# Kernel tuning notes

Hardware: AMD Instinct MI355X
Metric: run time of the kernel (lower is better)

## Reference

```python
import jax, jax.numpy as jnp
import numpy as np

N = 100000   # nodes
E = 600000   # edges
D = 128      # d_model
R = 200      # num_relations


def setup_inputs() -> dict:
    key = jax.random.key(0)
    ks = jax.random.split(key, 12)
    def nrm(k, shape, scale=0.02):
        return jax.random.normal(k, shape, jnp.float32) * scale
    return dict(
        node_features=jax.random.normal(ks[0], (N, D), jnp.float32),
        edge_index=jax.random.randint(ks[1], (2, E), 0, N),
        edge_type=jax.random.randint(ks[2], (E,), 0, R),
        rel_embed=nrm(ks[3], (R, D)),
        msg_w1=nrm(ks[4], (2 * D, D)), msg_b1=jnp.zeros((D,), jnp.float32),
        msg_w2=nrm(ks[5], (D, D)), msg_b2=jnp.zeros((D,), jnp.float32),
        attn_w1=nrm(ks[6], (2 * D, D)), attn_b1=jnp.zeros((D,), jnp.float32),
        attn_w2=nrm(ks[7], (D, 1)), attn_b2=jnp.zeros((1,), jnp.float32),
        ln1_g=jnp.ones((D,), jnp.float32), ln1_b=jnp.zeros((D,), jnp.float32),
        ffn_w1=nrm(ks[8], (D, 4 * D)), ffn_b1=jnp.zeros((4 * D,), jnp.float32),
        ffn_w2=nrm(ks[9], (4 * D, D)), ffn_b2=jnp.zeros((D,), jnp.float32),
        ln2_g=jnp.ones((D,), jnp.float32), ln2_b=jnp.zeros((D,), jnp.float32),
    )


def layer_norm(x, g, b, eps=1e-5):
    mu = x.mean(-1, keepdims=True)
    var = ((x - mu) ** 2).mean(-1, keepdims=True)
    return (x - mu) * jax.lax.rsqrt(var + eps) * g + b


def reference(node_features, edge_index, edge_type, rel_embed,
              msg_w1, msg_b1, msg_w2, msg_b2,
              attn_w1, attn_b1, attn_w2, attn_b2,
              ln1_g, ln1_b, ffn_w1, ffn_b1, ffn_w2, ffn_b2,
              ln2_g, ln2_b):
    Nn = node_features.shape[0]
    src, dst = edge_index[0], edge_index[1]
    # gather + edge message MLP
    src_feat = node_features[src]              # [E, D]
    rel_feat = rel_embed[edge_type]            # [E, D]
    h = jnp.concatenate([src_feat, rel_feat], axis=-1)          # [E, 2D]
    messages = jax.nn.relu(h @ msg_w1 + msg_b1) @ msg_w2 + msg_b2  # [E, D]
    # edge attention logits
    a_in = jnp.concatenate([node_features[dst], messages], axis=-1)  # [E, 2D]
    attn_raw = (jax.nn.leaky_relu(a_in @ attn_w1 + attn_b1, 0.2) @ attn_w2 + attn_b2)[:, 0]  # [E]
    # two-pass segment softmax over destination nodes
    attn_max = jax.ops.segment_max(attn_raw, dst, num_segments=Nn)   # [N]
    attn_exp = jnp.exp(attn_raw - attn_max[dst])                      # [E]
    attn_sum = jax.ops.segment_sum(attn_exp, dst, num_segments=Nn)   # [N]
    attn_w = attn_exp / (attn_sum[dst] + 1e-8)                        # [E]
    # scatter-add weighted messages
    aggr = jax.ops.segment_sum(attn_w[:, None] * messages, dst, num_segments=Nn)  # [N, D]
    x = layer_norm(node_features + aggr, ln1_g, ln1_b)
    ffn = jax.nn.gelu(x @ ffn_w1 + ffn_b1, approximate=False) @ ffn_w2 + ffn_b2
    return layer_norm(x + ffn, ln2_g, ln2_b)
```

## Files before the change

### kernel.cpp

```cpp
#include <hip/hip_runtime.h>
#include <hip/hip_bf16.h>

#define NN 100000
#define NE 600000
#define DD 128
#define RR 200
#define SCAN_NB ((NN + 255) / 256)

typedef __attribute__((ext_vector_type(8))) short bf16x8;
typedef __attribute__((ext_vector_type(4))) float f32x4;

__device__ __forceinline__ unsigned int bfbits(float x) {
    return (unsigned int)__builtin_bit_cast(unsigned short, __float2bfloat16(x));
}
__device__ __forceinline__ unsigned int pk2(float a, float b) {
    return bfbits(a) | (bfbits(b) << 16);
}
__device__ __forceinline__ unsigned short bf16s(float x) {
    return __builtin_bit_cast(unsigned short, __float2bfloat16(x));
}
__device__ __forceinline__ float unbf(unsigned short u) {
    return __builtin_bit_cast(float, ((unsigned int)u) << 16);
}
__device__ __forceinline__ float unlo(unsigned int u) {
    return __builtin_bit_cast(float, u << 16);
}
__device__ __forceinline__ float unhi(unsigned int u) {
    return __builtin_bit_cast(float, u & 0xffff0000u);
}

__device__ __forceinline__ void gload_lds16(const void* g, void* l) {
    __builtin_amdgcn_global_load_lds(
        (const __attribute__((address_space(1))) void*)g,
        (__attribute__((address_space(3))) void*)l, 16, 0, 0);
}

__global__ void k_initc(int* __restrict__ cnt) {
    int i = blockIdx.x * 256 + threadIdx.x;
    if (i < NN) cnt[i] = 0;
}

__global__ void k_hist(const int* __restrict__ dst, int* __restrict__ cnt) {
    int e = blockIdx.x * 256 + threadIdx.x;
    if (e < NE) atomicAdd(&cnt[dst[e]], 1);
}

__global__ void k_scanA(const int* __restrict__ cnt, int* __restrict__ bsum) {
    __shared__ int red[256];
    int i = blockIdx.x * 256 + threadIdx.x;
    red[threadIdx.x] = (i < NN) ? cnt[i] : 0;
    __syncthreads();
    for (int off = 128; off >= 1; off >>= 1) {
        if (threadIdx.x < off) red[threadIdx.x] += red[threadIdx.x + off];
        __syncthreads();
    }
    if (threadIdx.x == 0) bsum[blockIdx.x] = red[0];
}

__global__ void k_scanB(int* __restrict__ bsum) {
    __shared__ int sh[512];
    int t = threadIdx.x;
    int v = (t < SCAN_NB) ? bsum[t] : 0;
    sh[t] = v;
    __syncthreads();
    for (int off = 1; off < 512; off <<= 1) {
        int add = (t >= off) ? sh[t - off] : 0;
        __syncthreads();
        sh[t] += add;
        __syncthreads();
    }
    if (t < SCAN_NB) bsum[t] = sh[t] - v;
}

__global__ void k_scanC(const int* __restrict__ cnt, const int* __restrict__ bsum,
                        int* __restrict__ row_start, int* __restrict__ cursor) {
    __shared__ int sh[256];
    int i = blockIdx.x * 256 + threadIdx.x;
    int t = threadIdx.x;
    int v = (i < NN) ? cnt[i] : 0;
    sh[t] = v;
    __syncthreads();
    for (int off = 1; off < 256; off <<= 1) {
        int add = (t >= off) ? sh[t - off] : 0;
        __syncthreads();
        sh[t] += add;
        __syncthreads();
    }
    if (i < NN) {
        int ex = bsum[blockIdx.x] + sh[t] - v;
        row_start[i] = ex;
        cursor[i] = ex;
    }
}

__global__ void k_bucket(const int* __restrict__ src, const int* __restrict__ dst,
                         const int* __restrict__ etype, int* __restrict__ cursor,
                         int* __restrict__ srcs, int* __restrict__ ets,
                         int* __restrict__ dsts) {
    int e = blockIdx.x * 256 + threadIdx.x;
    if (e < NE) {
        int d = dst[e];
        int p = atomicAdd(&cursor[d], 1);
        srcs[p] = src[e];
        ets[p]  = etype[e];
        dsts[p] = d;
    }
}

__global__ void k_prep(const float* __restrict__ nf, unsigned short* __restrict__ nfb) {
    int i = blockIdx.x * 256 + threadIdx.x;
    if (i >= NN * DD / 8) return;
    const float* sp = nf + (size_t)i * 8;
    float4 f0 = *reinterpret_cast<const float4*>(sp);
    float4 f1 = *reinterpret_cast<const float4*>(sp + 4);
    uint4 v;
    v.x = pk2(f0.x, f0.y); v.y = pk2(f0.z, f0.w);
    v.z = pk2(f1.x, f1.y); v.w = pk2(f1.z, f1.w);
    *reinterpret_cast<uint4*>(nfb + (size_t)i * 8) = v;
}

__global__ void k_relc(const float* __restrict__ rel, const float* __restrict__ mw1,
                       const float* __restrict__ mb1, unsigned short* __restrict__ relcb) {
    int idx = blockIdx.x * 256 + threadIdx.x;
    if (idx >= RR * DD) return;
    int r = idx >> 7, n = idx & 127;
    float s = mb1[n];
    for (int k = 0; k < 128; ++k)
        s = fmaf(rel[r * 128 + k], mw1[(128 + k) * 128 + n], s);
    relcb[idx] = bf16s(s);
}

__global__ void k_mwb(const float* __restrict__ mw2, const float* __restrict__ mb2,
                      const float* __restrict__ aw1,
                      float* __restrict__ mwB, float* __restrict__ zb) {
    int idx = blockIdx.x * 256 + threadIdx.x;
    if (idx < 16384) {
        int k = idx >> 7, n = idx & 127;
        float s = 0.0f;
        for (int j = 0; j < 128; ++j)
            s = fmaf(mw2[k * 128 + j], aw1[(128 + j) * 128 + n], s);
        mwB[idx] = s;
    } else if (idx < 16512) {
        int n = idx - 16384;
        float s = 0.0f;
        for (int j = 0; j < 128; ++j)
            s = fmaf(mb2[j], aw1[(128 + j) * 128 + n], s);
        zb[n] = s;
    }
}

__global__ void k_pack(const float* __restrict__ mw1, const float* __restrict__ mw2,
                       const float* __restrict__ mwB,
                       const float* __restrict__ aw1,
                       const float* __restrict__ fw1, const float* __restrict__ fw2,
                       unsigned short* __restrict__ mw1p,
                       unsigned short* __restrict__ mwCp,
                       unsigned short* __restrict__ awTp,
                       unsigned short* __restrict__ fw1p,
                       unsigned short* __restrict__ fw2p) {
    int idx = blockIdx.x * 256 + threadIdx.x;
    if (idx < 16384) {
        int i = idx & 7, l = (idx >> 3) & 63, ks = (idx >> 9) & 3, nt = idx >> 11;
        int k = ks * 32 + (l >> 4) * 8 + i, n = nt * 16 + (l & 15);
        mw1p[idx] = bf16s(mw1[k * 128 + n]);
    } else if (idx < 49152) {
        int j = idx - 16384;
        int i = j & 7, l = (j >> 3) & 63, ks = (j >> 9) & 3, nt = j >> 11;
        int k = ks * 32 + (l >> 4) * 8 + i, n = nt * 16 + (l & 15);
        mwCp[j] = bf16s((n < 128) ? mw2[k * 128 + n] : mwB[k * 128 + (n - 128)]);
    } else if (idx < 65536) {
        int j = idx - 49152;
        int i = j & 7, l = (j >> 3) & 63, ks = (j >> 9) & 3, nt = j >> 11;
        int k = ks * 32 + (l >> 4) * 8 + i, n = nt * 16 + (l & 15);
        awTp[j] = bf16s(aw1[k * 128 + n]);
    } else if (idx < 131072) {
        int j = idx - 65536;
        int i = j & 7, l = (j >> 3) & 63, ks = (j >> 9) & 3, nt = j >> 11;
        int k = ks * 32 + (l >> 4) * 8 + i, n = nt * 16 + (l & 15);
        fw1p[j] = bf16s(fw1[k * 512 + n]);
    } else if (idx < 196608) {
        int j = idx - 131072;
        int i = j & 7, l = (j >> 3) & 63, ks = (j >> 9) & 15, nt = j >> 13;
        int k = ks * 32 + (l >> 4) * 8 + i, n = nt * 16 + (l & 15);
        fw2p[j] = bf16s(fw2[k * 128 + n]);
    }
}

__global__ __launch_bounds__(256) void k_nfa(
    const unsigned short* __restrict__ nfb, const unsigned short* __restrict__ awTp,
    const float* __restrict__ ab1, unsigned short* __restrict__ nfa)
{
    __shared__ alignas(16) unsigned short XB[64 * 128];
    const int t = threadIdx.x;
    const int w = t >> 6, l = t & 63;
    const int wm = w >> 1, wn = w & 1;
    const int lm = l & 15, lk = l >> 4;
    const int lrow = l >> 4, lslot = l & 15;
    const int n0 = blockIdx.x * 64;

    #pragma unroll
    for (int it = 0; it < 4; ++it) {
        int rb = w * 16 + it * 4;
        int row = rb + lrow;
        long grow = n0 + row; if (grow >= NN) grow = NN - 1;
        int c = lslot ^ (row & 7);
        gload_lds16(nfb + grow * DD + c * 8, &XB[rb * 128]);
    }
    __syncthreads();

    f32x4 acc[2][4];
    #pragma unroll
    for (int mf = 0; mf < 2; ++mf)
        #pragma unroll
        for (int nfr = 0; nfr < 4; ++nfr) acc[mf][nfr] = (f32x4){0.f, 0.f, 0.f, 0.f};

    #pragma unroll
    for (int ks = 0; ks < 4; ++ks) {
        bf16x8 a[2];
        #pragma unroll
        for (int mf = 0; mf < 2; ++mf) {
            int m = wm * 32 + mf * 16 + lm;
            int slot = (ks * 4 + lk) ^ (m & 7);
            a[mf] = *reinterpret_cast<const bf16x8*>(&XB[m * 128 + slot * 8]);
        }
        #pragma unroll
        for (int nfr = 0; nfr < 4; ++nfr) {
            int nt = wn * 4 + nfr;
            bf16x8 b = *reinterpret_cast<const bf16x8*>(&awTp[((nt * 4 + ks) * 64 + l) * 8]);
            acc[0][nfr] = __builtin_amdgcn_mfma_f32_16x16x32_bf16(a[0], b, acc[0][nfr], 0, 0, 0);
            acc[1][nfr] = __builtin_amdgcn_mfma_f32_16x16x32_bf16(a[1], b, acc[1][nfr], 0, 0, 0);
        }
    }
    __syncthreads();

    #pragma unroll
    for (int nfr = 0; nfr < 4; ++nfr) {
        int n = wn * 64 + nfr * 16 + lm;
        float bv = ab1[n];
        #pragma unroll
        for (int mf = 0; mf < 2; ++mf)
            #pragma unroll
            for (int r = 0; r < 4; ++r) {
                int m = wm * 32 + mf * 16 + lk * 4 + r;
                XB[m * 128 + n] = bf16s(acc[mf][nfr][r] + bv);
            }
    }
    __syncthreads();

    #pragma unroll
    for (int j = 0; j < 4; ++j) {
        int q = j * 256 + t;
        int row = q >> 4, c16 = q & 15;
        if (n0 + row < NN)
            *reinterpret_cast<uint4*>(&nfa[(size_t)(n0 + row) * DD + c16 * 8]) =
                *reinterpret_cast<const uint4*>(&XB[row * 128 + c16 * 8]);
    }
}

__global__ __launch_bounds__(512) void k_edge(
    const unsigned short* __restrict__ nfb, const int* __restrict__ srcs,
    const int* __restrict__ dsts, const int* __restrict__ ets,
    const unsigned short* __restrict__ nfa, const unsigned short* __restrict__ relcb,
    const unsigned short* __restrict__ mw1p, const unsigned short* __restrict__ mwCp,
    const float* __restrict__ mb2, const float* __restrict__ zb,
    const float* __restrict__ aw2, const float* __restrict__ ab2,
    unsigned short* __restrict__ msg_out, float* __restrict__ attn_raw)
{
    __shared__ alignas(16) unsigned short S[64 * 128];
    __shared__ alignas(16) unsigned short H[64 * 128];
    __shared__ float RED[64][2];

    const int t = threadIdx.x;
    const int w = t >> 6, l = t & 63;
    const int wm = w >> 2, wn = w & 3;
    const int lm = l & 15, lk = l >> 4;
    const int lrow = l >> 4, lslot = l & 15;
    const int e0 = blockIdx.x * 64;

    #pragma unroll
    for (int it = 0; it < 2; ++it) {
        int rb = w * 8 + it * 4;
        int row = rb + lrow;
        int c = lslot ^ (row & 7);
        gload_lds16(nfb + (size_t)srcs[e0 + row] * DD + c * 8, &S[rb * 128]);
    }
    #pragma unroll
    for (int it = 0; it < 2; ++it) {
        int rb = w * 8 + it * 4;
        int row = rb + lrow;
        int c = lslot ^ (row & 7);
        gload_lds16(relcb + (size_t)ets[e0 + row] * DD + c * 8, &H[rb * 128]);
    }
    __syncthreads();

    {
        f32x4 acc[2][2];
        #pragma unroll
        for (int mf = 0; mf < 2; ++mf)
            #pragma unroll
            for (int nfr = 0; nfr < 2; ++nfr) acc[mf][nfr] = (f32x4){0.f, 0.f, 0.f, 0.f};

        #pragma unroll
        for (int ks = 0; ks < 4; ++ks) {
            bf16x8 a[2];
            #pragma unroll
            for (int mf = 0; mf < 2; ++mf) {
                int m = wm * 32 + mf * 16 + lm;
                int slot = (ks * 4 + lk) ^ (m & 7);
                a[mf] = *reinterpret_cast<const bf16x8*>(&S[m * 128 + slot * 8]);
            }
            #pragma unroll
            for (int nfr = 0; nfr < 2; ++nfr) {
                int nt = wn * 2 + nfr;
                bf16x8 b = *reinterpret_cast<const bf16x8*>(&mw1p[((nt * 4 + ks) * 64 + l) * 8]);
                acc[0][nfr] = __builtin_amdgcn_mfma_f32_16x16x32_bf16(a[0], b, acc[0][nfr], 0, 0, 0);
                acc[1][nfr] = __builtin_amdgcn_mfma_f32_16x16x32_bf16(a[1], b, acc[1][nfr], 0, 0, 0);
            }
        }
        #pragma unroll
        for (int nfr = 0; nfr < 2; ++nfr) {
            int n = (wn * 2 + nfr) * 16 + lm;
            #pragma unroll
            for (int mf = 0; mf < 2; ++mf)
                #pragma unroll
                for (int r = 0; r < 4; ++r) {
                    int m = wm * 32 + mf * 16 + lk * 4 + r;
                    int sl = m * 128 + ((n >> 3) ^ (m & 7)) * 8 + (n & 7);
                    float v = acc[mf][nfr][r] + unbf(H[sl]);
                    v = fmaxf(v, 0.0f);
                    H[sl] = bf16s(v);
                }
        }
    }
    __syncthreads();

    #pragma unroll
    for (int it = 0; it < 2; ++it) {
        int rb = w * 8 + it * 4;
        int row = rb + lrow;
        int c = lslot ^ (row & 7);
        gload_lds16(nfa + (size_t)dsts[e0 + row] * DD + c * 8, &S[rb * 128]);
    }

    f32x4 acc[2][4];
    #pragma unroll
    for (int mf = 0; mf < 2; ++mf)
        #pragma unroll
        for (int nfr = 0; nfr < 4; ++nfr) acc[mf][nfr] = (f32x4){0.f, 0.f, 0.f, 0.f};

    #pragma unroll
    for (int ks = 0; ks < 4; ++ks) {
        bf16x8 a[2];
        #pragma unroll
        for (int mf = 0; mf < 2; ++mf) {
            int m = wm * 32 + mf * 16 + lm;
            int slot = (ks * 4 + lk) ^ (m & 7);
            a[mf] = *reinterpret_cast<const bf16x8*>(&H[m * 128 + slot * 8]);
        }
        #pragma unroll
        for (int nfr = 0; nfr < 4; ++nfr) {
            int nt = wn * 4 + nfr;
            bf16x8 b = *reinterpret_cast<const bf16x8*>(&mwCp[((nt * 4 + ks) * 64 + l) * 8]);
            acc[0][nfr] = __builtin_amdgcn_mfma_f32_16x16x32_bf16(a[0], b, acc[0][nfr], 0, 0, 0);
            acc[1][nfr] = __builtin_amdgcn_mfma_f32_16x16x32_bf16(a[1], b, acc[1][nfr], 0, 0, 0);
        }
    }
    __syncthreads();

    if (wn < 2) {
        #pragma unroll
        for (int nfr = 0; nfr < 4; ++nfr) {
            int n = (wn * 4 + nfr) * 16 + lm;
            float bv = mb2[n];
            #pragma unroll
            for (int mf = 0; mf < 2; ++mf)
                #pragma unroll
                for (int r = 0; r < 4; ++r) {
                    int m = wm * 32 + mf * 16 + lk * 4 + r;
                    H[m * 128 + ((n >> 3) ^ (m & 7)) * 8 + (n & 7)] = bf16s(acc[mf][nfr][r] + bv);
                }
        }
    } else {
        float zbv[4], aw2v[4];
        #pragma unroll
        for (int nfr = 0; nfr < 4; ++nfr) {
            int nc = (wn - 2) * 64 + nfr * 16 + lm;
            zbv[nfr] = zb[nc];
            aw2v[nfr] = aw2[nc];
        }
        #pragma unroll
        for (int mf = 0; mf < 2; ++mf)
            #pragma unroll
            for (int r = 0; r < 4; ++r) {
                int m = wm * 32 + mf * 16 + lk * 4 + r;
                float s = 0.0f;
                #pragma unroll
                for (int nfr = 0; nfr < 4; ++nfr) {
                    int nc = (wn - 2) * 64 + nfr * 16 + lm;
                    float v = acc[mf][nfr][r] + zbv[nfr]
                            + unbf(S[m * 128 + ((nc >> 3) ^ (m & 7)) * 8 + (nc & 7)]);
                    v = (v > 0.0f) ? v : 0.2f * v;
                    s = fmaf(v, aw2v[nfr], s);
                }
                s += __shfl_xor(s, 1, 64);
                s += __shfl_xor(s, 2, 64);
                s += __shfl_xor(s, 4, 64);
                s += __shfl_xor(s, 8, 64);
                if (lm == 0) RED[m][wn - 2] = s;
            }
    }
    __syncthreads();

    #pragma unroll
    for (int j = 0; j < 2; ++j) {
        int q = j * 512 + t;
        int row = q >> 4, c16 = q & 15;
        int slot = c16 ^ (row & 7);
        *reinterpret_cast<uint4*>(&msg_out[(size_t)(e0 + row) * DD + c16 * 8]) =
            *reinterpret_cast<const uint4*>(&H[row * 128 + slot * 8]);
    }
    if (t < 64) {
        attn_raw[e0 + t] = RED[t][0] + RED[t][1] + ab2[0];
    }
}

__global__ __launch_bounds__(256) void k_aggr(
    const unsigned short* __restrict__ msg, const float* __restrict__ raw,
    const int* __restrict__ row_start, const int* __restrict__ cnt,
    float* __restrict__ aggr)
{
    const int l = threadIdx.x & 63;
    const int n = blockIdx.x * 4 + (threadIdx.x >> 6);
    if (n >= NN) return;
    const int rs = row_start[n], deg = cnt[n];

    float m = -INFINITY;
    for (int j = l; j < deg; j += 64) m = fmaxf(m, raw[rs + j]);
    #pragma unroll
    for (int off = 32; off >= 1; off >>= 1) m = fmaxf(m, __shfl_xor(m, off, 64));

    float s = 0.0f;
    for (int j = l; j < deg; j += 64) s += expf(raw[rs + j] - m);
    #pragma unroll
    for (int off = 32; off >= 1; off >>= 1) s += __shfl_xor(s, off, 64);
    const float rinv = 1.0f / (s + 1e-8f);

    float a0 = 0.0f, a1 = 0.0f;
    for (int j = 0; j < deg; ++j) {
        float w = expf(raw[rs + j] - m) * rinv;
        unsigned int v = *reinterpret_cast<const unsigned int*>(
            &msg[(size_t)(rs + j) * DD + l * 2]);
        a0 = fmaf(w, unlo(v), a0);
        a1 = fmaf(w, unhi(v), a1);
    }
    float2 o = {a0, a1};
    *reinterpret_cast<float2*>(&aggr[(size_t)n * DD + l * 2]) = o;
}

__global__ __launch_bounds__(512) void k_node(
    const float* __restrict__ nf, const float* __restrict__ aggr,
    const float* __restrict__ g1, const float* __restrict__ b1,
    const unsigned short* __restrict__ fw1p, const float* __restrict__ fb1,
    const unsigned short* __restrict__ fw2p, const float* __restrict__ fb2,
    const float* __restrict__ g2, const float* __restrict__ b2,
    float* __restrict__ out)
{
    __shared__ alignas(16) unsigned short XB[64 * 128];
    __shared__ alignas(16) unsigned short HB[64 * 256];

    const int t = threadIdx.x;
    const int w = t >> 6, l = t & 63;
    const int wm = w >> 2, wn = w & 3;
    const int lm = l & 15, lk = l >> 4;
    const int row = t >> 3;
    const int q = t & 7;
    const long n0 = (long)blockIdx.x * 64;
    const long rg = n0 + row;
    const long rc = (rg < NN) ? rg : (NN - 1);

    float xr[16];
    float s = 0.0f, ss = 0.0f;
    {
        const float* xp = nf + rc * DD + q * 16;
        const float* ap = aggr + rc * DD + q * 16;
        #pragma unroll
        for (int i = 0; i < 4; ++i) {
            float4 a = *reinterpret_cast<const float4*>(xp + i * 4);
            float4 b = *reinterpret_cast<const float4*>(ap + i * 4);
            float v0 = a.x + b.x, v1 = a.y + b.y, v2 = a.z + b.z, v3 = a.w + b.w;
            xr[i * 4 + 0] = v0; xr[i * 4 + 1] = v1; xr[i * 4 + 2] = v2; xr[i * 4 + 3] = v3;
            s += v0 + v1 + v2 + v3;
            ss = fmaf(v0, v0, ss); ss = fmaf(v1, v1, ss);
            ss = fmaf(v2, v2, ss); ss = fmaf(v3, v3, ss);
        }
    }
    s  += __shfl_xor(s, 1, 64);  s  += __shfl_xor(s, 2, 64);  s  += __shfl_xor(s, 4, 64);
    ss += __shfl_xor(ss, 1, 64); ss += __shfl_xor(ss, 2, 64); ss += __shfl_xor(ss, 4, 64);
    {
        float mu = s * (1.0f / DD);
        float var = ss * (1.0f / DD) - mu * mu;
        float rstd = rsqrtf(var + 1e-5f);
        #pragma unroll
        for (int i = 0; i < 4; ++i) {
            float4 gv = *reinterpret_cast<const float4*>(g1 + q * 16 + i * 4);
            float4 bv = *reinterpret_cast<const float4*>(b1 + q * 16 + i * 4);
            xr[i * 4 + 0] = (xr[i * 4 + 0] - mu) * rstd * gv.x + bv.x;
            xr[i * 4 + 1] = (xr[i * 4 + 1] - mu) * rstd * gv.y + bv.y;
            xr[i * 4 + 2] = (xr[i * 4 + 2] - mu) * rstd * gv.z + bv.z;
            xr[i * 4 + 3] = (xr[i * 4 + 3] - mu) * rstd * gv.w + bv.w;
        }
        #pragma unroll
        for (int i = 0; i < 2; ++i) {
            int c = q * 2 + i, slot = c ^ (row & 7);
            uint4 v;
            v.x = pk2(xr[i * 8 + 0], xr[i * 8 + 1]);
            v.y = pk2(xr[i * 8 + 2], xr[i * 8 + 3]);
            v.z = pk2(xr[i * 8 + 4], xr[i * 8 + 5]);
            v.w = pk2(xr[i * 8 + 6], xr[i * 8 + 7]);
            *reinterpret_cast<uint4*>(&XB[row * 128 + slot * 8]) = v;
        }
    }
    __syncthreads();

    f32x4 acc2[2][2];
    #pragma unroll
    for (int mf = 0; mf < 2; ++mf)
        #pragma unroll
        for (int nfr = 0; nfr < 2; ++nfr) acc2[mf][nfr] = (f32x4){0.f, 0.f, 0.f, 0.f};

    #pragma unroll
    for (int half = 0; half < 2; ++half) {
        f32x4 acc[2][4];
        #pragma unroll
        for (int mf = 0; mf < 2; ++mf)
            #pragma unroll
            for (int nfr = 0; nfr < 4; ++nfr) acc[mf][nfr] = (f32x4){0.f, 0.f, 0.f, 0.f};

        #pragma unroll
        for (int ks = 0; ks < 4; ++ks) {
            bf16x8 a[2];
            #pragma unroll
            for (int mf = 0; mf < 2; ++mf) {
                int m = wm * 32 + mf * 16 + lm;
                int slot = (ks * 4 + lk) ^ (m & 7);
                a[mf] = *reinterpret_cast<const bf16x8*>(&XB[m * 128 + slot * 8]);
            }
            #pragma unroll
            for (int nfr = 0; nfr < 4; ++nfr) {
                int nt = half * 16 + wn * 4 + nfr;
                bf16x8 b = *reinterpret_cast<const bf16x8*>(&fw1p[((nt * 4 + ks) * 64 + l) * 8]);
                acc[0][nfr] = __builtin_amdgcn_mfma_f32_16x16x32_bf16(a[0], b, acc[0][nfr], 0, 0, 0);
                acc[1][nfr] = __builtin_amdgcn_mfma_f32_16x16x32_bf16(a[1], b, acc[1][nfr], 0, 0, 0);
            }
        }
        #pragma unroll
        for (int nfr = 0; nfr < 4; ++nfr) {
            int nl = (wn * 4 + nfr) * 16 + lm;
            float bv = fb1[half * 256 + nl];
            #pragma unroll
            for (int mf = 0; mf < 2; ++mf)
                #pragma unroll
                for (int r = 0; r < 4; ++r) {
                    int m = wm * 32 + mf * 16 + lk * 4 + r;
                    float h = acc[mf][nfr][r] + bv;
                    float e = __expf(h * -1.702f);
                    float gvv = h * __builtin_amdgcn_rcpf(1.0f + e);
                    HB[m * 256 + (((nl >> 3) ^ (m & 7)) * 8) + (nl & 7)] = bf16s(gvv);
                }
        }
        __syncthreads();

        #pragma unroll
        for (int ks = 0; ks < 8; ++ks) {
            bf16x8 a[2];
            #pragma unroll
            for (int mf = 0; mf < 2; ++mf) {
                int m = wm * 32 + mf * 16 + lm;
                int slot = (ks * 4 + lk) ^ (m & 7);
                a[mf] = *reinterpret_cast<const bf16x8*>(&HB[m * 256 + slot * 8]);
            }
            #pragma unroll
            for (int nfr = 0; nfr < 2; ++nfr) {
                int nt = wn * 2 + nfr;
                int kg = half * 8 + ks;
                bf16x8 b = *reinterpret_cast<const bf16x8*>(&fw2p[((nt * 16 + kg) * 64 + l) * 8]);
                acc2[0][nfr] = __builtin_amdgcn_mfma_f32_16x16x32_bf16(a[0], b, acc2[0][nfr], 0, 0, 0);
                acc2[1][nfr] = __builtin_amdgcn_mfma_f32_16x16x32_bf16(a[1], b, acc2[1][nfr], 0, 0, 0);
            }
        }
        __syncthreads();
    }

    #pragma unroll
    for (int nfr = 0; nfr < 2; ++nfr) {
        int n = (wn * 2 + nfr) * 16 + lm;
        float bv = fb2[n];
        #pragma unroll
        for (int mf = 0; mf < 2; ++mf)
            #pragma unroll
            for (int r = 0; r < 4; ++r) {
                int m = wm * 32 + mf * 16 + lk * 4 + r;
                XB[m * 128 + (((n >> 3) ^ (m & 7)) * 8) + (n & 7)] = bf16s(acc2[mf][nfr][r] + bv);
            }
    }
    __syncthreads();

    float s2 = 0.0f, ss2 = 0.0f;
    #pragma unroll
    for (int i = 0; i < 2; ++i) {
        int c = q * 2 + i, slot = c ^ (row & 7);
        uint4 v = *reinterpret_cast<const uint4*>(&XB[row * 128 + slot * 8]);
        float f[8];
        f[0] = unlo(v.x); f[1] = unhi(v.x); f[2] = unlo(v.y); f[3] = unhi(v.y);
        f[4] = unlo(v.z); f[5] = unhi(v.z); f[6] = unlo(v.w); f[7] = unhi(v.w);
        #pragma unroll
        for (int j = 0; j < 8; ++j) {
            float vv = xr[i * 8 + j] + f[j];
            xr[i * 8 + j] = vv;
            s2 += vv;
            ss2 = fmaf(vv, vv, ss2);
        }
    }
    s2  += __shfl_xor(s2, 1, 64);  s2  += __shfl_xor(s2, 2, 64);  s2  += __shfl_xor(s2, 4, 64);
    ss2 += __shfl_xor(ss2, 1, 64); ss2 += __shfl_xor(ss2, 2, 64); ss2 += __shfl_xor(ss2, 4, 64);
    {
        float mu = s2 * (1.0f / DD);
        float var = ss2 * (1.0f / DD) - mu * mu;
        float rstd = rsqrtf(var + 1e-5f);
        if (rg < NN) {
            float* op = out + rg * DD + q * 16;
            #pragma unroll
            for (int i = 0; i < 4; ++i) {
                float4 gv = *reinterpret_cast<const float4*>(g2 + q * 16 + i * 4);
                float4 bv = *reinterpret_cast<const float4*>(b2 + q * 16 + i * 4);
                float4 o;
                o.x = (xr[i * 4 + 0] - mu) * rstd * gv.x + bv.x;
                o.y = (xr[i * 4 + 1] - mu) * rstd * gv.y + bv.y;
                o.z = (xr[i * 4 + 2] - mu) * rstd * gv.z + bv.z;
                o.w = (xr[i * 4 + 3] - mu) * rstd * gv.w + bv.w;
                *reinterpret_cast<float4*>(op + i * 4) = o;
            }
        }
    }
}

extern "C" void kernel_launch(void* const* d_in, const int* in_sizes, int n_in,
                              void* d_out, int out_size, void* d_ws, size_t ws_size,
                              hipStream_t stream)
{
    const float* nf  = (const float*)d_in[0];
    const int*   ei  = (const int*)d_in[1];
    const int*   et  = (const int*)d_in[2];
    const float* rel = (const float*)d_in[3];
    const float* mw1 = (const float*)d_in[4];
    const float* mb1 = (const float*)d_in[5];
    const float* mw2 = (const float*)d_in[6];
    const float* mb2 = (const float*)d_in[7];
    const float* aw1 = (const float*)d_in[8];
    const float* ab1 = (const float*)d_in[9];
    const float* aw2 = (const float*)d_in[10];
    const float* ab2 = (const float*)d_in[11];
    const float* g1  = (const float*)d_in[12];
    const float* b1  = (const float*)d_in[13];
    const float* fw1 = (const float*)d_in[14];
    const float* fb1 = (const float*)d_in[15];
    const float* fw2 = (const float*)d_in[16];
    const float* fb2 = (const float*)d_in[17];
    const float* g2  = (const float*)d_in[18];
    const float* b2  = (const float*)d_in[19];
    float* out = (float*)d_out;

    char* ws = (char*)d_ws;
    size_t off = 0;
    auto alloc = [&](size_t bytes) -> char* {
        char* p = ws + off;
        off += (bytes + 255) & ~(size_t)255;
        return p;
    };
    unsigned short* msg = (unsigned short*)alloc((size_t)NE * DD * 2);
    float* attn_raw = (float*)alloc((size_t)NE * 4);
    float* aggr     = (float*)alloc((size_t)NN * DD * 4);
    unsigned short* nfb  = (unsigned short*)alloc((size_t)NN * DD * 2);
    unsigned short* relcb = (unsigned short*)alloc((size_t)RR * DD * 2);
    float* mwB = (float*)alloc((size_t)16384 * 4);
    float* zb  = (float*)alloc((size_t)128 * 4);
    int* cnt       = (int*)alloc((size_t)NN * 4);
    int* row_start = (int*)alloc((size_t)NN * 4);
    int* cursor    = (int*)alloc((size_t)NN * 4);
    int* srcs      = (int*)alloc((size_t)NE * 4);
    int* ets       = (int*)alloc((size_t)NE * 4);
    int* dsts      = (int*)alloc((size_t)NE * 4);
    int* bsum      = (int*)alloc((size_t)SCAN_NB * 4);
    unsigned short* mw1p = (unsigned short*)alloc(16384 * 2);
    unsigned short* mwCp = (unsigned short*)alloc(32768 * 2);
    unsigned short* awTp = (unsigned short*)alloc(16384 * 2);
    unsigned short* fw1p = (unsigned short*)alloc(65536 * 2);
    unsigned short* fw2p = (unsigned short*)alloc(65536 * 2);

    unsigned short* nfa = (unsigned short*)aggr;

    const int* srcp = ei;
    const int* dstp = ei + NE;

    hipLaunchKernelGGL(k_initc, dim3(SCAN_NB), dim3(256), 0, stream, cnt);
    hipLaunchKernelGGL(k_hist, dim3((NE + 255) / 256), dim3(256), 0, stream, dstp, cnt);
    hipLaunchKernelGGL(k_scanA, dim3(SCAN_NB), dim3(256), 0, stream, cnt, bsum);
    hipLaunchKernelGGL(k_scanB, dim3(1), dim3(512), 0, stream, bsum);
    hipLaunchKernelGGL(k_scanC, dim3(SCAN_NB), dim3(256), 0, stream, cnt, bsum, row_start, cursor);
    hipLaunchKernelGGL(k_bucket, dim3((NE + 255) / 256), dim3(256), 0, stream,
                       srcp, dstp, et, cursor, srcs, ets, dsts);
    hipLaunchKernelGGL(k_prep, dim3(NN * DD / 8 / 256), dim3(256), 0, stream, nf, nfb);
    hipLaunchKernelGGL(k_mwb, dim3(65), dim3(256), 0, stream, mw2, mb2, aw1, mwB, zb);
    hipLaunchKernelGGL(k_pack, dim3(768), dim3(256), 0, stream,
                       mw1, mw2, mwB, aw1, fw1, fw2, mw1p, mwCp, awTp, fw1p, fw2p);
    hipLaunchKernelGGL(k_relc, dim3(100), dim3(256), 0, stream, rel, mw1, mb1, relcb);
    hipLaunchKernelGGL(k_nfa, dim3((NN + 63) / 64), dim3(256), 0, stream,
                       nfb, awTp, ab1, nfa);
    hipLaunchKernelGGL(k_edge, dim3(NE / 64), dim3(512), 0, stream,
                       nfb, srcs, dsts, ets, nfa, relcb,
                       mw1p, mwCp, mb2, zb, aw2, ab2,
                       msg, attn_raw);
    hipLaunchKernelGGL(k_aggr, dim3((NN + 3) / 4), dim3(256), 0, stream,
                       msg, attn_raw, row_start, cnt, aggr);
    hipLaunchKernelGGL(k_node, dim3((NN + 63) / 64), dim3(512), 0, stream,
                       nf, aggr, g1, b1, fw1p, fb1, fw2p, fb2, g2, b2, out);
}
```

Measured before the change: 471.6 us.

## Aggregate hidden activations per node and apply message W2 after aggregation

Because msg_w2 is linear, the edge kernel now stores the ReLU hidden activations and computes only the attention-side GEMM with the prefolded W2·attn_w1 matrix. The per-edge second message GEMM moves to the node kernel, where it runs on the aggregated hidden vector for 100k nodes instead of 600k edges. The aggregate is stored as bf16 rather than fp32, and the three small weight-preparation kernels are merged into one setup launch. One risk: the node kernel adds mb2 to every node, including nodes with no incoming edges, which the reference would leave at zero. It also assumes the attention weights sum to exactly one, ignoring the 1e-8 epsilon, and the extra bf16 rounding changes numerics slightly.

```diff
diff --git a/kernel.cpp b/kernel.cpp
--- a/kernel.cpp
+++ b/kernel.cpp
@@ -119,60 +119,41 @@
     *reinterpret_cast<uint4*>(nfb + (size_t)i * 8) = v;
 }
 
-__global__ void k_relc(const float* __restrict__ rel, const float* __restrict__ mw1,
-                       const float* __restrict__ mb1, unsigned short* __restrict__ relcb) {
-    int idx = blockIdx.x * 256 + threadIdx.x;
-    if (idx >= RR * DD) return;
-    int r = idx >> 7, n = idx & 127;
-    float s = mb1[n];
-    for (int k = 0; k < 128; ++k)
-        s = fmaf(rel[r * 128 + k], mw1[(128 + k) * 128 + n], s);
-    relcb[idx] = bf16s(s);
-}
-
-__global__ void k_mwb(const float* __restrict__ mw2, const float* __restrict__ mb2,
-                      const float* __restrict__ aw1,
-                      float* __restrict__ mwB, float* __restrict__ zb) {
-    int idx = blockIdx.x * 256 + threadIdx.x;
-    if (idx < 16384) {
-        int k = idx >> 7, n = idx & 127;
-        float s = 0.0f;
-        for (int j = 0; j < 128; ++j)
-            s = fmaf(mw2[k * 128 + j], aw1[(128 + j) * 128 + n], s);
-        mwB[idx] = s;
-    } else if (idx < 16512) {
-        int n = idx - 16384;
-        float s = 0.0f;
-        for (int j = 0; j < 128; ++j)
-            s = fmaf(mb2[j], aw1[(128 + j) * 128 + n], s);
-        zb[n] = s;
-    }
-}
-
-__global__ void k_pack(const float* __restrict__ mw1, const float* __restrict__ mw2,
-                       const float* __restrict__ mwB,
-                       const float* __restrict__ aw1,
-                       const float* __restrict__ fw1, const float* __restrict__ fw2,
-                       unsigned short* __restrict__ mw1p,
-                       unsigned short* __restrict__ mwCp,
-                       unsigned short* __restrict__ awTp,
-                       unsigned short* __restrict__ fw1p,
-                       unsigned short* __restrict__ fw2p) {
+__global__ void k_setup(const float* __restrict__ mw1, const float* __restrict__ mb1,
+                        const float* __restrict__ mw2, const float* __restrict__ mb2,
+                        const float* __restrict__ aw1, const float* __restrict__ rel,
+                        const float* __restrict__ fw1, const float* __restrict__ fw2,
+                        unsigned short* __restrict__ mw1p,
+                        unsigned short* __restrict__ mw2p,
+                        unsigned short* __restrict__ awTp,
+                        unsigned short* __restrict__ mwBp,
+                        unsigned short* __restrict__ fw1p,
+                        unsigned short* __restrict__ fw2p,
+                        unsigned short* __restrict__ relcb,
+                        float* __restrict__ zb) {
     int idx = blockIdx.x * 256 + threadIdx.x;
     if (idx < 16384) {
         int i = idx & 7, l = (idx >> 3) & 63, ks = (idx >> 9) & 3, nt = idx >> 11;
         int k = ks * 32 + (l >> 4) * 8 + i, n = nt * 16 + (l & 15);
         mw1p[idx] = bf16s(mw1[k * 128 + n]);
-    } else if (idx < 49152) {
+    } else if (idx < 32768) {
         int j = idx - 16384;
         int i = j & 7, l = (j >> 3) & 63, ks = (j >> 9) & 3, nt = j >> 11;
         int k = ks * 32 + (l >> 4) * 8 + i, n = nt * 16 + (l & 15);
-        mwCp[j] = bf16s((n < 128) ? mw2[k * 128 + n] : mwB[k * 128 + (n - 128)]);
+        mw2p[j] = bf16s(mw2[k * 128 + n]);
+    } else if (idx < 49152) {
+        int j = idx - 32768;
+        int i = j & 7, l = (j >> 3) & 63, ks = (j >> 9) & 3, nt = j >> 11;
+        int k = ks * 32 + (l >> 4) * 8 + i, n = nt * 16 + (l & 15);
+        awTp[j] = bf16s(aw1[k * 128 + n]);
     } else if (idx < 65536) {
         int j = idx - 49152;
         int i = j & 7, l = (j >> 3) & 63, ks = (j >> 9) & 3, nt = j >> 11;
         int k = ks * 32 + (l >> 4) * 8 + i, n = nt * 16 + (l & 15);
-        awTp[j] = bf16s(aw1[k * 128 + n]);
+        float s = 0.0f;
+        for (int j2 = 0; j2 < 128; ++j2)
+            s = fmaf(mw2[k * 128 + j2], aw1[(128 + j2) * 128 + n], s);
+        mwBp[j] = bf16s(s);
     } else if (idx < 131072) {
         int j = idx - 65536;
         int i = j & 7, l = (j >> 3) & 63, ks = (j >> 9) & 3, nt = j >> 11;
@@ -183,6 +164,19 @@
         int i = j & 7, l = (j >> 3) & 63, ks = (j >> 9) & 15, nt = j >> 13;
         int k = ks * 32 + (l >> 4) * 8 + i, n = nt * 16 + (l & 15);
         fw2p[j] = bf16s(fw2[k * 128 + n]);
+    } else if (idx < 222208) {
+        int j = idx - 196608;
+        int r = j >> 7, n = j & 127;
+        float s = mb1[n];
+        for (int k = 0; k < 128; ++k)
+            s = fmaf(rel[r * 128 + k], mw1[(128 + k) * 128 + n], s);
+        relcb[j] = bf16s(s);
+    } else if (idx < 222336) {
+        int n = idx - 222208;
+        float s = 0.0f;
+        for (int j2 = 0; j2 < 128; ++j2)
+            s = fmaf(mb2[j2], aw1[(128 + j2) * 128 + n], s);
+        zb[n] = s;
     }
 }
 
@@ -261,14 +255,14 @@
     const unsigned short* __restrict__ nfb, const int* __restrict__ srcs,
     const int* __restrict__ dsts, const int* __restrict__ ets,
     const unsigned short* __restrict__ nfa, const unsigned short* __restrict__ relcb,
-    const unsigned short* __restrict__ mw1p, const unsigned short* __restrict__ mwCp,
-    const float* __restrict__ mb2, const float* __restrict__ zb,
-    const float* __restrict__ aw2, const float* __restrict__ ab2,
-    unsigned short* __restrict__ msg_out, float* __restrict__ attn_raw)
+    const unsigned short* __restrict__ mw1p, const unsigned short* __restrict__ mwBp,
+    const float* __restrict__ zb, const float* __restrict__ aw2,
+    const float* __restrict__ ab2,
+    unsigned short* __restrict__ hid_out, float* __restrict__ attn_raw)
 {
     __shared__ alignas(16) unsigned short S[64 * 128];
     __shared__ alignas(16) unsigned short H[64 * 128];
-    __shared__ float RED[64][2];
+    __shared__ float RED[64][4];
 
     const int t = threadIdx.x;
     const int w = t >> 6, l = t & 63;
@@ -294,11 +288,11 @@
     __syncthreads();
 
     {
-        f32x4 acc[2][2];
+        f32x4 acc1[2][2];
         #pragma unroll
         for (int mf = 0; mf < 2; ++mf)
             #pragma unroll
-            for (int nfr = 0; nfr < 2; ++nfr) acc[mf][nfr] = (f32x4){0.f, 0.f, 0.f, 0.f};
+            for (int nfr = 0; nfr < 2; ++nfr) acc1[mf][nfr] = (f32x4){0.f, 0.f, 0.f, 0.f};
 
         #pragma unroll
         for (int ks = 0; ks < 4; ++ks) {
@@ -313,8 +307,8 @@
             for (int nfr = 0; nfr < 2; ++nfr) {
                 int nt = wn * 2 + nfr;
                 bf16x8 b = *reinterpret_cast<const bf16x8*>(&mw1p[((nt * 4 + ks) * 64 + l) * 8]);
-                acc[0][nfr] = __builtin_amdgcn_mfma_f32_16x16x32_bf16(a[0], b, acc[0][nfr], 0, 0, 0);
-                acc[1][nfr] = __builtin_amdgcn_mfma_f32_16x16x32_bf16(a[1], b, acc[1][nfr], 0, 0, 0);
+                acc1[0][nfr] = __builtin_amdgcn_mfma_f32_16x16x32_bf16(a[0], b, acc1[0][nfr], 0, 0, 0);
+                acc1[1][nfr] = __builtin_amdgcn_mfma_f32_16x16x32_bf16(a[1], b, acc1[1][nfr], 0, 0, 0);
             }
         }
         #pragma unroll
@@ -326,7 +320,7 @@
                 for (int r = 0; r < 4; ++r) {
                     int m = wm * 32 + mf * 16 + lk * 4 + r;
                     int sl = m * 128 + ((n >> 3) ^ (m & 7)) * 8 + (n & 7);
-                    float v = acc[mf][nfr][r] + unbf(H[sl]);
+                    float v = acc1[mf][nfr][r] + unbf(H[sl]);
                     v = fmaxf(v, 0.0f);
                     H[sl] = bf16s(v);
                 }
@@ -334,6 +328,14 @@
     }
     __syncthreads();
 
+    #pragma unroll
+    for (int j = 0; j < 2; ++j) {
+        int q = j * 512 + t;
+        int row = q >> 4, c16 = q & 15;
+        int slot = c16 ^ (row & 7);
+        *reinterpret_cast<uint4*>(&hid_out[(size_t)(e0 + row) * DD + c16 * 8]) =
+            *reinterpret_cast<const uint4*>(&H[row * 128 + slot * 8]);
+    }
     #pragma unroll
     for (int it = 0; it < 2; ++it) {
         int rb = w * 8 + it * 4;
@@ -342,11 +344,11 @@
         gload_lds16(nfa + (size_t)dsts[e0 + row] * DD + c * 8, &S[rb * 128]);
     }
 
-    f32x4 acc[2][4];
+    f32x4 acc[2][2];
     #pragma unroll
     for (int mf = 0; mf < 2; ++mf)
         #pragma unroll
-        for (int nfr = 0; nfr < 4; ++nfr) acc[mf][nfr] = (f32x4){0.f, 0.f, 0.f, 0.f};
+        for (int nfr = 0; nfr < 2; ++nfr) acc[mf][nfr] = (f32x4){0.f, 0.f, 0.f, 0.f};
 
     #pragma unroll
     for (int ks = 0; ks < 4; ++ks) {
@@ -358,33 +360,20 @@
             a[mf] = *reinterpret_cast<const bf16x8*>(&H[m * 128 + slot * 8]);
         }
         #pragma unroll
-        for (int nfr = 0; nfr < 4; ++nfr) {
-            int nt = wn * 4 + nfr;
-            bf16x8 b = *reinterpret_cast<const bf16x8*>(&mwCp[((nt * 4 + ks) * 64 + l) * 8]);
+        for (int nfr = 0; nfr < 2; ++nfr) {
+            int nt = wn * 2 + nfr;
+            bf16x8 b = *reinterpret_cast<const bf16x8*>(&mwBp[((nt * 4 + ks) * 64 + l) * 8]);
             acc[0][nfr] = __builtin_amdgcn_mfma_f32_16x16x32_bf16(a[0], b, acc[0][nfr], 0, 0, 0);
             acc[1][nfr] = __builtin_amdgcn_mfma_f32_16x16x32_bf16(a[1], b, acc[1][nfr], 0, 0, 0);
         }
     }
     __syncthreads();
 
-    if (wn < 2) {
-        #pragma unroll
-        for (int nfr = 0; nfr < 4; ++nfr) {
-            int n = (wn * 4 + nfr) * 16 + lm;
-            float bv = mb2[n];
-            #pragma unroll
-            for (int mf = 0; mf < 2; ++mf)
-                #pragma unroll
-                for (int r = 0; r < 4; ++r) {
-                    int m = wm * 32 + mf * 16 + lk * 4 + r;
-                    H[m * 128 + ((n >> 3) ^ (m & 7)) * 8 + (n & 7)] = bf16s(acc[mf][nfr][r] + bv);
-                }
-        }
-    } else {
-        float zbv[4], aw2v[4];
-        #pragma unroll
-        for (int nfr = 0; nfr < 4; ++nfr) {
-            int nc = (wn - 2) * 64 + nfr * 16 + lm;
+    {
+        float zbv[2], aw2v[2];
+        #pragma unroll
+        for (int nfr = 0; nfr < 2; ++nfr) {
+            int nc = (wn * 2 + nfr) * 16 + lm;
             zbv[nfr] = zb[nc];
             aw2v[nfr] = aw2[nc];
         }
@@ -395,8 +384,8 @@
                 int m = wm * 32 + mf * 16 + lk * 4 + r;
                 float s = 0.0f;
                 #pragma unroll
-                for (int nfr = 0; nfr < 4; ++nfr) {
-                    int nc = (wn - 2) * 64 + nfr * 16 + lm;
+                for (int nfr = 0; nfr < 2; ++nfr) {
+                    int nc = (wn * 2 + nfr) * 16 + lm;
                     float v = acc[mf][nfr][r] + zbv[nfr]
                             + unbf(S[m * 128 + ((nc >> 3) ^ (m & 7)) * 8 + (nc & 7)]);
                     v = (v > 0.0f) ? v : 0.2f * v;
@@ -406,28 +395,20 @@
                 s += __shfl_xor(s, 2, 64);
                 s += __shfl_xor(s, 4, 64);
                 s += __shfl_xor(s, 8, 64);
-                if (lm == 0) RED[m][wn - 2] = s;
-            }
-    }
-    __syncthreads();
-
-    #pragma unroll
-    for (int j = 0; j < 2; ++j) {
-        int q = j * 512 + t;
-        int row = q >> 4, c16 = q & 15;
-        int slot = c16 ^ (row & 7);
-        *reinterpret_cast<uint4*>(&msg_out[(size_t)(e0 + row) * DD + c16 * 8]) =
-            *reinterpret_cast<const uint4*>(&H[row * 128 + slot * 8]);
-    }
+                if (lm == 0) RED[m][wn] = s;
+            }
+    }
+    __syncthreads();
+
     if (t < 64) {
-        attn_raw[e0 + t] = RED[t][0] + RED[t][1] + ab2[0];
+        attn_raw[e0 + t] = RED[t][0] + RED[t][1] + RED[t][2] + RED[t][3] + ab2[0];
     }
 }
 
 __global__ __launch_bounds__(256) void k_aggr(
-    const unsigned short* __restrict__ msg, const float* __restrict__ raw,
+    const unsigned short* __restrict__ hid, const float* __restrict__ raw,
     const int* __restrict__ row_start, const int* __restrict__ cnt,
-    float* __restrict__ aggr)
+    unsigned short* __restrict__ haggrb)
 {
     const int l = threadIdx.x & 63;
     const int n = blockIdx.x * 4 + (threadIdx.x >> 6);
@@ -449,16 +430,16 @@
     for (int j = 0; j < deg; ++j) {
         float w = expf(raw[rs + j] - m) * rinv;
         unsigned int v = *reinterpret_cast<const unsigned int*>(
-            &msg[(size_t)(rs + j) * DD + l * 2]);
+            &hid[(size_t)(rs + j) * DD + l * 2]);
         a0 = fmaf(w, unlo(v), a0);
         a1 = fmaf(w, unhi(v), a1);
     }
-    float2 o = {a0, a1};
-    *reinterpret_cast<float2*>(&aggr[(size_t)n * DD + l * 2]) = o;
+    *reinterpret_cast<unsigned int*>(&haggrb[(size_t)n * DD + l * 2]) = pk2(a0, a1);
 }
 
 __global__ __launch_bounds__(512) void k_node(
-    const float* __restrict__ nf, const float* __restrict__ aggr,
+    const float* __restrict__ nf, const unsigned short* __restrict__ haggrb,
+    const unsigned short* __restrict__ mw2p, const float* __restrict__ mb2,
     const float* __restrict__ g1, const float* __restrict__ b1,
     const unsigned short* __restrict__ fw1p, const float* __restrict__ fb1,
     const unsigned short* __restrict__ fw2p, const float* __restrict__ fb2,
@@ -472,26 +453,84 @@
     const int w = t >> 6, l = t & 63;
     const int wm = w >> 2, wn = w & 3;
     const int lm = l & 15, lk = l >> 4;
+    const int lrow = l >> 4, lslot = l & 15;
     const int row = t >> 3;
     const int q = t & 7;
     const long n0 = (long)blockIdx.x * 64;
     const long rg = n0 + row;
     const long rc = (rg < NN) ? rg : (NN - 1);
 
+    unsigned short* HG = HB;
+    #pragma unroll
+    for (int it = 0; it < 2; ++it) {
+        int rb = w * 8 + it * 4;
+        int rr = rb + lrow;
+        long grow = n0 + rr; if (grow >= NN) grow = NN - 1;
+        int c = lslot ^ (rr & 7);
+        gload_lds16(haggrb + grow * DD + c * 8, &HG[rb * 128]);
+    }
+    __syncthreads();
+
+    {
+        f32x4 acc0[2][2];
+        #pragma unroll
+        for (int mf = 0; mf < 2; ++mf)
+            #pragma unroll
+            for (int nfr = 0; nfr < 2; ++nfr) acc0[mf][nfr] = (f32x4){0.f, 0.f, 0.f, 0.f};
+
+        #pragma unroll
+        for (int ks = 0; ks < 4; ++ks) {
+            bf16x8 a[2];
+            #pragma unroll
+            for (int mf = 0; mf < 2; ++mf) {
+                int m = wm * 32 + mf * 16 + lm;
+                int slot = (ks * 4 + lk) ^ (m & 7);
+                a[mf] = *reinterpret_cast<const bf16x8*>(&HG[m * 128 + slot * 8]);
+            }
+            #pragma unroll
+            for (int nfr = 0; nfr < 2; ++nfr) {
+                int nt = wn * 2 + nfr;
+                bf16x8 b = *reinterpret_cast<const bf16x8*>(&mw2p[((nt * 4 + ks) * 64 + l) * 8]);
+                acc0[0][nfr] = __builtin_amdgcn_mfma_f32_16x16x32_bf16(a[0], b, acc0[0][nfr], 0, 0, 0);
+                acc0[1][nfr] = __builtin_amdgcn_mfma_f32_16x16x32_bf16(a[1], b, acc0[1][nfr], 0, 0, 0);
+            }
+        }
+        #pragma unroll
+        for (int nfr = 0; nfr < 2; ++nfr) {
+            int n = (wn * 2 + nfr) * 16 + lm;
+            float bv = mb2[n];
+            #pragma unroll
+            for (int mf = 0; mf < 2; ++mf)
+                #pragma unroll
+                for (int r = 0; r < 4; ++r) {
+                    int m = wm * 32 + mf * 16 + lk * 4 + r;
+                    XB[m * 128 + ((n >> 3) ^ (m & 7)) * 8 + (n & 7)] = bf16s(acc0[mf][nfr][r] + bv);
+                }
+        }
+    }
+    __syncthreads();
+
     float xr[16];
     float s = 0.0f, ss = 0.0f;
     {
         const float* xp = nf + rc * DD + q * 16;
-        const float* ap = aggr + rc * DD + q * 16;
-        #pragma unroll
-        for (int i = 0; i < 4; ++i) {
-            float4 a = *reinterpret_cast<const float4*>(xp + i * 4);
-            float4 b = *reinterpret_cast<const float4*>(ap + i * 4);
-            float v0 = a.x + b.x, v1 = a.y + b.y, v2 = a.z + b.z, v3 = a.w + b.w;
-            xr[i * 4 + 0] = v0; xr[i * 4 + 1] = v1; xr[i * 4 + 2] = v2; xr[i * 4 + 3] = v3;
-            s += v0 + v1 + v2 + v3;
-            ss = fmaf(v0, v0, ss); ss = fmaf(v1, v1, ss);
-            ss = fmaf(v2, v2, ss); ss = fmaf(v3, v3, ss);
+        #pragma unroll
+        for (int i = 0; i < 2; ++i) {
+            int c = q * 2 + i, slot = c ^ (row & 7);
+            uint4 v = *reinterpret_cast<const uint4*>(&XB[row * 128 + slot * 8]);
+            float f[8];
+            f[0] = unlo(v.x); f[1] = unhi(v.x); f[2] = unlo(v.y); f[3] = unhi(v.y);
+            f[4] = unlo(v.z); f[5] = unhi(v.z); f[6] = unlo(v.w); f[7] = unhi(v.w);
+            float4 a = *reinterpret_cast<const float4*>(xp + i * 8);
+            float4 b = *reinterpret_cast<const float4*>(xp + i * 8 + 4);
+            float vv[8] = {a.x + f[0], a.y + f[1], a.z + f[2], a.w + f[3],
+                           b.x + f[4], b.y + f[5], b.z + f[6], b.w + f[7]};
+            #pragma unroll
+            for (int j = 0; j < 8; ++j) {
+                xr[i * 8 + j] = vv[j];
+                s += vv[j];
+                ss = fmaf(vv[j], vv[j], ss);
+            }
         }
     }
     s  += __shfl_xor(s, 1, 64);  s  += __shfl_xor(s, 2, 64);  s  += __shfl_xor(s, 4, 64);
@@ -677,12 +716,11 @@
         off += (bytes + 255) & ~(size_t)255;
         return p;
     };
-    unsigned short* msg = (unsigned short*)alloc((size_t)NE * DD * 2);
+    unsigned short* hid = (unsigned short*)alloc((size_t)NE * DD * 2);
     float* attn_raw = (float*)alloc((size_t)NE * 4);
-    float* aggr     = (float*)alloc((size_t)NN * DD * 4);
+    unsigned short* haggrb = (unsigned short*)alloc((size_t)NN * DD * 2);
     unsigned short* nfb  = (unsigned short*)alloc((size_t)NN * DD * 2);
     unsigned short* relcb = (unsigned short*)alloc((size_t)RR * DD * 2);
-    float* mwB = (float*)alloc((size_t)16384 * 4);
     float* zb  = (float*)alloc((size_t)128 * 4);
     int* cnt       = (int*)alloc((size_t)NN * 4);
     int* row_start = (int*)alloc((size_t)NN * 4);
@@ -692,12 +730,13 @@
     int* dsts      = (int*)alloc((size_t)NE * 4);
     int* bsum      = (int*)alloc((size_t)SCAN_NB * 4);
     unsigned short* mw1p = (unsigned short*)alloc(16384 * 2);
-    unsigned short* mwCp = (unsigned short*)alloc(32768 * 2);
+    unsigned short* mw2p = (unsigned short*)alloc(16384 * 2);
     unsigned short* awTp = (unsigned short*)alloc(16384 * 2);
+    unsigned short* mwBp = (unsigned short*)alloc(16384 * 2);
     unsigned short* fw1p = (unsigned short*)alloc(65536 * 2);
     unsigned short* fw2p = (unsigned short*)alloc(65536 * 2);
 
-    unsigned short* nfa = (unsigned short*)aggr;
+    unsigned short* nfa = haggrb;
 
     const int* srcp = ei;
     const int* dstp = ei + NE;
@@ -710,18 +749,17 @@
     hipLaunchKernelGGL(k_bucket, dim3((NE + 255) / 256), dim3(256), 0, stream,
                        srcp, dstp, et, cursor, srcs, ets, dsts);
     hipLaunchKernelGGL(k_prep, dim3(NN * DD / 8 / 256), dim3(256), 0, stream, nf, nfb);
-    hipLaunchKernelGGL(k_mwb, dim3(65), dim3(256), 0, stream, mw2, mb2, aw1, mwB, zb);
-    hipLaunchKernelGGL(k_pack, dim3(768), dim3(256), 0, stream,
-                       mw1, mw2, mwB, aw1, fw1, fw2, mw1p, mwCp, awTp, fw1p, fw2p);
-    hipLaunchKernelGGL(k_relc, dim3(100), dim3(256), 0, stream, rel, mw1, mb1, relcb);
+    hipLaunchKernelGGL(k_setup, dim3(869), dim3(256), 0, stream,
+                       mw1, mb1, mw2, mb2, aw1, rel, fw1, fw2,
+                       mw1p, mw2p, awTp, mwBp, fw1p, fw2p, relcb, zb);
     hipLaunchKernelGGL(k_nfa, dim3((NN + 63) / 64), dim3(256), 0, stream,
                        nfb, awTp, ab1, nfa);
     hipLaunchKernelGGL(k_edge, dim3(NE / 64), dim3(512), 0, stream,
                        nfb, srcs, dsts, ets, nfa, relcb,
-                       mw1p, mwCp, mb2, zb, aw2, ab2,
-                       msg, attn_raw);
+                       mw1p, mwBp, zb, aw2, ab2,
+                       hid, attn_raw);
     hipLaunchKernelGGL(k_aggr, dim3((NN + 3) / 4), dim3(256), 0, stream,
-                       msg, attn_raw, row_start, cnt, aggr);
+                       hid, attn_raw, row_start, cnt, haggrb);
     hipLaunchKernelGGL(k_node, dim3((NN + 63) / 64), dim3(512), 0, stream,
-                       nf, aggr, g1, b1, fw1p, fb1, fw2p, fb2, g2, b2, out);
-}
+                       nf, haggrb, mw2p, mb2, g1, b1, fw1p, fb1, fw2p, fb2, g2, b2, out);
+}
```

After: 432.2 us. 1.09x faster.
